# Optimization experiments

Measured on AMD Instinct MI355X. Metric: run time of the kernel, lower is better.

## Reference

```python
import jax, jax.numpy as jnp
import numpy as np

N_POINTS = 32
N_HEADS = 4
EMBED = 256
TAU = 2.0


def _grid_sample_bilinear(val, gx, gy):
    # val: [N, C, H, W]; gx, gy: [N, Q, P] normalized coords in [-1, 1]
    # bilinear, padding_mode='zeros', align_corners=False
    N, C, H, W = val.shape
    ix = (gx + 1.0) * (W * 0.5) - 0.5
    iy = (gy + 1.0) * (H * 0.5) - 0.5
    x0 = jnp.floor(ix)
    y0 = jnp.floor(iy)
    x1 = x0 + 1.0
    y1 = y0 + 1.0
    wx1 = ix - x0
    wx0 = 1.0 - wx1
    wy1 = iy - y0
    wy0 = 1.0 - wy1
    gather = jax.vmap(lambda v, yy, xx: v[:, yy, xx])  # per-image advanced-index gather
    out = jnp.zeros((N, C) + gx.shape[1:], dtype=val.dtype)
    for xs, ys, wx, wy in ((x0, y0, wx0, wy0), (x1, y0, wx1, wy0),
                           (x0, y1, wx0, wy1), (x1, y1, wx1, wy1)):
        m = ((xs >= 0) & (xs < W) & (ys >= 0) & (ys < H)).astype(val.dtype) * wx * wy
        xi = jnp.clip(xs, 0, W - 1).astype(jnp.int32)
        yi = jnp.clip(ys, 0, H - 1).astype(jnp.int32)
        out = out + gather(val, yi, xi) * m[:, None]
    return out  # [N, C, Q, P]


def setup_inputs() -> dict:
    key = jax.random.key(0)
    ks = jax.random.split(key, 18)
    B, L = 2, 1000
    lvl_hw = [(256, 256), (128, 128), (64, 64), (32, 32)]
    inp = {}
    for i, (h, w) in enumerate(lvl_hw):
        inp[f'value{i}'] = jax.random.normal(ks[i], (B, EMBED, h, w), jnp.float32)
    inp['query_content'] = jax.random.normal(ks[4], (B, L, EMBED), jnp.float32)
    img = 1024.0
    xy = jax.random.uniform(ks[5], (B, L, 2), minval=0.0, maxval=img)
    z = jax.random.uniform(ks[6], (B, L, 1), minval=4.0, maxval=6.5)
    r = jax.random.uniform(ks[7], (B, L, 1), minval=-0.8, maxval=0.8)
    th = jax.random.uniform(ks[8], (B, L, 1), minval=-np.pi, maxval=np.pi)
    inp['query_xyzrt'] = jnp.concatenate([xy, z, r, th], axis=-1).astype(jnp.float32)
    inp['strides'] = jnp.array([4, 8, 16, 32], jnp.int32)
    s = 0.02
    inp['W_off'] = jax.random.normal(ks[9], (EMBED, N_HEADS * N_POINTS * 3)) * s
    inp['b_off'] = jax.random.normal(ks[10], (N_HEADS * N_POINTS * 3,)) * 0.2
    inp['W_ca1'] = jax.random.normal(ks[11], (EMBED, EMBED // 4)) * s
    inp['W_ca2'] = jax.random.normal(ks[12], (EMBED // 4, EMBED)) * s
    inp['W_sa1'] = jax.random.normal(ks[13], (EMBED, EMBED // 4)) * s
    inp['W_sa2'] = jax.random.normal(ks[14], (EMBED // 4, N_HEADS * N_POINTS)) * s
    inp['W_out'] = jax.random.normal(ks[15], (EMBED * N_POINTS, EMBED)) * s
    inp['b_out'] = jnp.zeros((EMBED,), jnp.float32)
    return inp


def reference(value0, value1, value2, value3, query_content, query_xyzrt, strides,
              W_off, b_off, W_ca1, W_ca2, W_sa1, W_sa2, W_out, b_out):
    values = [value0, value1, value2, value3]
    B, L, _ = query_content.shape
    P = N_HEADS * N_POINTS
    G = N_HEADS
    ch = EMBED // G

    # ---- make_sample_points ----
    offset = (query_content @ W_off + b_off).reshape(B, L, P, 3)
    roi_cc = query_xyzrt[..., :2]                      # [B,L,2]
    scale = 2.0 ** query_xyzrt[..., 2:3]
    ratio = 2.0 ** jnp.concatenate([query_xyzrt[..., 3:4] * -0.5,
                                    query_xyzrt[..., 3:4] * 0.5], axis=-1)
    roi_wh = scale * ratio                             # [B,L,2]
    theta = query_xyzrt[..., 4]
    c, s = jnp.cos(theta), jnp.sin(theta)
    R = jnp.stack([jnp.stack([c, -s], -1), jnp.stack([s, c], -1)], -2)  # [B,L,2,2]
    off_xy = offset[..., :2] * roi_wh[:, :, None, :]
    rot_xy = jnp.einsum('blpj,blij->blpi', off_xy, R)  # offset @ R^T
    sample_xy = roi_cc[:, :, None, :] + rot_xy         # [B,L,P,2] absolute coords
    sample_z = query_xyzrt[..., 2][:, :, None] + offset[..., 2]  # [B,L,P]

    # ---- level weights: sigmoid(-(z - log2(stride))^2 / tau) ----
    grid = jnp.log2(strides.astype(sample_z.dtype))    # [n_levels]
    lvl_w = jax.nn.sigmoid(-((sample_z[..., None] - grid) ** 2) / TAU)  # [B,L,P,n_lvl]

    # ---- multi-level rotated deformable sampling ----
    sampling_value = jnp.zeros((B, L, G, N_POINTS, ch), query_content.dtype)
    for lvl, v in enumerate(values):
        H, W = v.shape[2], v.shape[3]
        stride_f = strides[lvl].astype(sample_xy.dtype)
        mapping = jnp.stack([W * stride_f, H * stride_f])  # (x_extent, y_extent)
        norm_xy = sample_xy / mapping * 2.0 - 1.0          # [B,L,P,2] in [-1,1]
        # split points into head groups: [B,L,G,pts,2] -> [B*G, L, pts, 2]
        g_xy = norm_xy.reshape(B, L, G, N_POINTS, 2).transpose(0, 2, 1, 3, 4).reshape(B * G, L, N_POINTS, 2)
        v_g = v.reshape(B * G, ch, H, W)
        out = _grid_sample_bilinear(v_g, g_xy[..., 0], g_xy[..., 1])  # [B*G, ch, L, pts]
        w = lvl_w[..., lvl].reshape(B, L, G, N_POINTS).transpose(0, 2, 1, 3).reshape(B * G, 1, L, N_POINTS)
        out = out * w
        sampling_value = sampling_value + out.reshape(B, G, ch, L, N_POINTS).transpose(0, 3, 1, 4, 2)

    # ---- channel / spatial attention gates ----
    ca = jax.nn.sigmoid(jax.nn.relu(query_content @ W_ca1) @ W_ca2)
    ca = ca.reshape(B, L, G, 1, ch)
    sa = jax.nn.sigmoid(jax.nn.relu(query_content @ W_sa1) @ W_sa2)
    sa = sa.reshape(B, L, G, N_POINTS, 1)
    out = sampling_value * ca * sa
    out = out.reshape(B, L, G * N_POINTS * ch) @ W_out + b_out
    return out + query_content
```

## Files before the change

### kernel.cpp

```cpp
#include <hip/hip_runtime.h>

#define NQ    2000
#define KDIM  8192
#define EMB   256
#define MPAD  2048
#define SPLITK 8

typedef __attribute__((ext_vector_type(8))) short bf16x8;
typedef __attribute__((ext_vector_type(4))) float f32x4;

__device__ __forceinline__ float sigf(float x) { return 1.0f / (1.0f + __expf(-x)); }

__device__ __forceinline__ unsigned short f2bf(float x) {
    union { float f; unsigned int u; } v; v.f = x;
    unsigned int r = v.u + 0x7fffu + ((v.u >> 16) & 1u);
    return (unsigned short)(r >> 16);
}
__device__ __forceinline__ float bf2f(unsigned short h) {
    union { unsigned int u; float f; } v; v.u = ((unsigned int)h) << 16; return v.f;
}

__global__ __launch_bounds__(256) void trans_kernel(
    const float* __restrict__ v0, const float* __restrict__ v1,
    const float* __restrict__ v2, const float* __restrict__ v3,
    unsigned short* __restrict__ vt0, unsigned short* __restrict__ vt1,
    unsigned short* __restrict__ vt2, unsigned short* __restrict__ vt3,
    const float* __restrict__ Wout, unsigned short* __restrict__ Wtb,
    const float* __restrict__ Woff, const float* __restrict__ Wca1,
    const float* __restrict__ Wsa1,
    unsigned short* __restrict__ WH, unsigned short* __restrict__ WL,
    const float* __restrict__ qc,
    unsigned short* __restrict__ qcH, unsigned short* __restrict__ qcL)
{
    __shared__ float tile[64][33];
    int bid = blockIdx.x;
    const int t = threadIdx.x;

    if (bid < 21760) {
        const float* v; unsigned short* vt; int H;
        if (bid < 16384)      { v = v0; vt = vt0; H = 256; }
        else if (bid < 20480) { bid -= 16384; v = v1; vt = vt1; H = 128; }
        else if (bid < 21504) { bid -= 20480; v = v2; vt = vt2; H = 64; }
        else                  { bid -= 21504; v = v3; vt = vt3; H = 32; }
        const int y  = bid % H;            bid /= H;
        const int xt = bid % (H >> 5);     bid /= (H >> 5);
        const int ct = bid & 3;
        const int b  = bid >> 2;
        const float* src = v + ((size_t)(b * 256 + ct * 64) * H + y) * H + xt * 32;
        const int xi = t & 31;
        #pragma unroll
        for (int i = 0; i < 8; i++) {
            const int c = (t >> 5) + i * 8;
            tile[c][xi] = src[(size_t)c * H * H + xi];
        }
        __syncthreads();
        unsigned short* dst = vt + (((size_t)(b * H + y) * H + xt * 32) * 256) + ct * 64;
        const int ci = (t & 31) * 2;
        #pragma unroll
        for (int i = 0; i < 4; i++) {
            const int x2 = (t >> 5) + i * 8;
            ushort2 pk;
            pk.x = f2bf(tile[ci][x2]);
            pk.y = f2bf(tile[ci + 1][x2]);
            *(ushort2*)(dst + (size_t)x2 * 256 + ci) = pk;
        }
    } else if (bid < 23808) {
        const int local = bid - 21760;
        const int k0 = (local & 255) * 32, n0 = (local >> 8) * 32;
        float (*tl)[33] = tile;
        #pragma unroll
        for (int i = 0; i < 4; i++) {
            const int ki = (t >> 5) + i * 8;
            tl[ki][t & 31] = Wout[(size_t)(k0 + ki) * 256 + n0 + (t & 31)];
        }
        __syncthreads();
        #pragma unroll
        for (int i = 0; i < 4; i++) {
            const int ni = (t >> 5) + i * 8;
            const int ki = t & 31;
            Wtb[(size_t)(n0 + ni) * KDIM + k0 + ki] = f2bf(tl[ki][ni]);
        }
    } else if (bid < 24320) {
        const int n = bid - 23808;
        float val;
        if (n < 384)      val = Woff[(size_t)t * 384 + n];
        else if (n < 448) val = Wca1[(size_t)t * 64 + (n - 384)];
        else              val = Wsa1[(size_t)t * 64 + (n - 448)];
        const unsigned short hh = f2bf(val);
        WH[(size_t)n * 256 + t] = hh;
        WL[(size_t)n * 256 + t] = f2bf(val - bf2f(hh));
    } else {
        const int q = bid - 24320;
        const float val = (q < NQ) ? qc[(size_t)q * 256 + t] : 0.f;
        const unsigned short hh = f2bf(val);
        qcH[(size_t)q * 256 + t] = hh;
        qcL[(size_t)q * 256 + t] = f2bf(val - bf2f(hh));
    }
}

__global__ __launch_bounds__(256) void gemmA_kernel(
    const unsigned short* __restrict__ qcH, const unsigned short* __restrict__ qcL,
    const unsigned short* __restrict__ WH,  const unsigned short* __restrict__ WL,
    float* __restrict__ Hout)
{
    const int m0 = blockIdx.x * 64;
    const int n0 = blockIdx.y * 64;
    const int t  = threadIdx.x;
    const int w    = t >> 6;
    const int lane = t & 63;
    const int mw = (w & 1) * 32;
    const int nw = (w >> 1) * 32;
    const int quad = lane >> 4;
    const int l16  = lane & 15;

    f32x4 acc[2][2] = {};
    #pragma unroll
    for (int pass = 0; pass < 3; pass++) {
        const unsigned short* Ap = (pass == 2) ? qcL : qcH;
        const unsigned short* Bp = (pass == 1) ? WL : WH;
        const unsigned short* ar0 = Ap + (size_t)(m0 + mw + l16) * 256 + quad * 8;
        const unsigned short* ar1 = ar0 + 16 * 256;
        const unsigned short* br0 = Bp + (size_t)(n0 + nw + l16) * 256 + quad * 8;
        const unsigned short* br1 = br0 + 16 * 256;
        #pragma unroll
        for (int k = 0; k < 256; k += 32) {
            const bf16x8 a0 = *(const bf16x8*)(ar0 + k);
            const bf16x8 a1 = *(const bf16x8*)(ar1 + k);
            const bf16x8 b0 = *(const bf16x8*)(br0 + k);
            const bf16x8 b1 = *(const bf16x8*)(br1 + k);
            acc[0][0] = __builtin_amdgcn_mfma_f32_16x16x32_bf16(a0, b0, acc[0][0], 0, 0, 0);
            acc[0][1] = __builtin_amdgcn_mfma_f32_16x16x32_bf16(a0, b1, acc[0][1], 0, 0, 0);
            acc[1][0] = __builtin_amdgcn_mfma_f32_16x16x32_bf16(a1, b0, acc[1][0], 0, 0, 0);
            acc[1][1] = __builtin_amdgcn_mfma_f32_16x16x32_bf16(a1, b1, acc[1][1], 0, 0, 0);
        }
    }
    #pragma unroll
    for (int i = 0; i < 2; i++)
        #pragma unroll
        for (int j = 0; j < 2; j++) {
            const int n = n0 + nw + 16 * j + l16;
            #pragma unroll
            for (int r = 0; r < 4; r++) {
                const int m = m0 + mw + 16 * i + quad * 4 + r;
                Hout[(size_t)m * 512 + n] = acc[i][j][r];
            }
        }
}

__global__ __launch_bounds__(256) void finish_kernel(
    const float* __restrict__ Hbuf, const float* __restrict__ xyzrt,
    const float* __restrict__ boff,
    const float* __restrict__ Wca2, const float* __restrict__ Wsa2,
    float* __restrict__ qdata)
{
    const int q0 = blockIdx.x * 8;
    const int t  = threadIdx.x;
    __shared__ float hca[8][64];
    __shared__ float hsa[8][64];
    __shared__ float sas[8][128];

    for (int i = t; i < 1024; i += 256) {
        const int q = i >> 7, j = i & 127;
        const float v = fmaxf(Hbuf[(size_t)(q0 + q) * 512 + 384 + j], 0.f);
        if (j < 64) hca[q][j] = v; else hsa[q][j - 64] = v;
    }
    __syncthreads();

    {
        float acc[8] = {};
        for (int j = 0; j < 64; j++) {
            const float wv = Wca2[(size_t)j * 256 + t];
            #pragma unroll
            for (int q = 0; q < 8; q++) acc[q] = fmaf(hca[q][j], wv, acc[q]);
        }
        #pragma unroll
        for (int q = 0; q < 8; q++)
            qdata[(size_t)(q0 + q) * 1024 + 768 + t] = sigf(acc[q]);
    }
    {
        const int c  = t & 127;
        const int qb = (t >> 7) * 4;
        float acc[4] = {};
        for (int j = 0; j < 64; j++) {
            const float wv = Wsa2[(size_t)j * 128 + c];
            #pragma unroll
            for (int qq = 0; qq < 4; qq++) acc[qq] = fmaf(hsa[qb + qq][j], wv, acc[qq]);
        }
        #pragma unroll
        for (int qq = 0; qq < 4; qq++) sas[qb + qq][c] = sigf(acc[qq]);
    }
    __syncthreads();

    {
        const int p  = t & 127;
        const int qb = (t >> 7) * 4;
        #pragma unroll
        for (int qq = 0; qq < 4; qq++) {
            const int q = qb + qq;
            const float* hrow = Hbuf + (size_t)(q0 + q) * 512 + p * 3;
            const float o0 = hrow[0] + boff[p * 3 + 0];
            const float o1 = hrow[1] + boff[p * 3 + 1];
            const float o2 = hrow[2] + boff[p * 3 + 2];
            const float* xr = xyzrt + (size_t)(q0 + q) * 5;
            const float x = xr[0], y = xr[1], z = xr[2], r = xr[3], th = xr[4];
            const float sc  = exp2f(z);
            const float rw  = sc * exp2f(-0.5f * r);
            const float rh  = sc * exp2f( 0.5f * r);
            const float cth = __cosf(th), sth = __sinf(th);
            const float ox = o0 * rw;
            const float oy = o1 * rh;
            float* qd = qdata + (size_t)(q0 + q) * 1024;
            qd[p]       = x + cth * ox - sth * oy;
            qd[128 + p] = y + sth * ox + cth * oy;
            const float sz = z + o2;
            const float sa = sas[q][p];
            #pragma unroll
            for (int l = 0; l < 4; l++) {
                const float d = sz - (float)(2 + l);
                qd[256 + p * 4 + l] = sigf(-0.5f * d * d) * sa;
            }
        }
    }
}

__global__ __launch_bounds__(256) void sample_kernel(
    const unsigned short* __restrict__ v0, const unsigned short* __restrict__ v1,
    const unsigned short* __restrict__ v2, const unsigned short* __restrict__ v3,
    const float* __restrict__ qdata,
    unsigned short* __restrict__ X)
{
    const int wid  = blockIdx.x * 4 + (threadIdx.x >> 6);
    const int lane = threadIdx.x & 63;
    const int q  = wid >> 4;
    const int pb = (wid & 15) * 8;
    const int pt = lane >> 3;
    const int gp = pb + pt;
    const int g  = gp >> 5;
    const int c8 = (lane & 7) * 8;
    const int b  = (q >= 1000) ? 1 : 0;

    const float* qd = qdata + (size_t)q * 1024;
    const float px = qd[gp];
    const float py = qd[128 + gp];
    float wlv[4];
    #pragma unroll
    for (int l = 0; l < 4; l++) wlv[l] = qd[256 + gp * 4 + l];

    const unsigned short* vals[4] = { v0, v1, v2, v3 };
    const int cbase = g * 64 + c8;

    float acc[8] = {};
    #pragma unroll
    for (int l = 0; l < 4; l++) {
        const int   H   = 256 >> l;
        const float inv = 1.0f / (float)(4 << l);
        const float wl  = wlv[l];
        const float ix = px * inv - 0.5f;
        const float iy = py * inv - 0.5f;
        const float x0f = floorf(ix), y0f = floorf(iy);
        const int   x0 = (int)x0f,    y0 = (int)y0f;
        const float fx1 = ix - x0f, fx0 = 1.f - fx1;
        const float fy1 = iy - y0f, fy0 = 1.f - fy1;
        const bool xi0 = (x0 >= 0) & (x0 < H);
        const bool xi1 = (x0 + 1 >= 0) & (x0 + 1 < H);
        const bool yi0 = (y0 >= 0) & (y0 < H);
        const bool yi1 = (y0 + 1 >= 0) & (y0 + 1 < H);
        const int xc0 = min(max(x0, 0), H - 1);
        const int xc1 = min(max(x0 + 1, 0), H - 1);
        const int yc0 = min(max(y0, 0), H - 1);
        const int yc1 = min(max(y0 + 1, 0), H - 1);
        const float m00 = (xi0 & yi0) ? wl * fx0 * fy0 : 0.f;
        const float m10 = (xi1 & yi0) ? wl * fx1 * fy0 : 0.f;
        const float m01 = (xi0 & yi1) ? wl * fx0 * fy1 : 0.f;
        const float m11 = (xi1 & yi1) ? wl * fx1 * fy1 : 0.f;

        const unsigned short* base = vals[l] + (size_t)b * H * H * 256 + cbase;
        const int ry0 = yc0 * H, ry1 = yc1 * H;
        const uint4 d00 = *(const uint4*)(base + (size_t)(ry0 + xc0) * 256);
        const uint4 d10 = *(const uint4*)(base + (size_t)(ry0 + xc1) * 256);
        const uint4 d01 = *(const uint4*)(base + (size_t)(ry1 + xc0) * 256);
        const uint4 d11 = *(const uint4*)(base + (size_t)(ry1 + xc1) * 256);

        const uint4 dv[4] = { d00, d10, d01, d11 };
        const float mv[4] = { m00, m10, m01, m11 };
        #pragma unroll
        for (int tap = 0; tap < 4; tap++) {
            const unsigned int du[4] = { dv[tap].x, dv[tap].y, dv[tap].z, dv[tap].w };
            const float m = mv[tap];
            #pragma unroll
            for (int i = 0; i < 4; i++) {
                union { unsigned int u; float f; } lo, hi;
                lo.u = du[i] << 16;
                hi.u = du[i] & 0xffff0000u;
                acc[2 * i]     = fmaf(m, lo.f, acc[2 * i]);
                acc[2 * i + 1] = fmaf(m, hi.f, acc[2 * i + 1]);
            }
        }
    }

    const float* caf = qd + 768 + cbase;
    const float4 ca0 = *(const float4*)caf;
    const float4 ca1 = *(const float4*)(caf + 4);
    const float cav[8] = { ca0.x, ca0.y, ca0.z, ca0.w, ca1.x, ca1.y, ca1.z, ca1.w };
    uint4 o;
    unsigned int* op = (unsigned int*)&o;
    #pragma unroll
    for (int i = 0; i < 4; i++) {
        const unsigned int lo = f2bf(acc[2 * i] * cav[2 * i]);
        const unsigned int hi = f2bf(acc[2 * i + 1] * cav[2 * i + 1]);
        op[i] = lo | (hi << 16);
    }
    *(uint4*)(X + (size_t)q * KDIM + pb * 64 + lane * 8) = o;
}

__global__ __launch_bounds__(256) void gemm_kernel(
    const unsigned short* __restrict__ X,
    const unsigned short* __restrict__ Wt,
    float* __restrict__ part)
{
    const int m0 = blockIdx.x * 64;
    const int n0 = blockIdx.y * 64;
    const int z  = blockIdx.z;
    const int t  = threadIdx.x;
    const int w    = t >> 6;
    const int lane = t & 63;
    const int mw = (w & 1) * 32;
    const int nw = (w >> 1) * 32;
    const int quad = lane >> 4;
    const int l16  = lane & 15;

    const unsigned short* ar0 = X  + (size_t)(m0 + mw + l16) * KDIM + quad * 8;
    const unsigned short* ar1 = ar0 + (size_t)16 * KDIM;
    const unsigned short* br0 = Wt + (size_t)(n0 + nw + l16) * KDIM + quad * 8;
    const unsigned short* br1 = br0 + (size_t)16 * KDIM;

    f32x4 acc[2][2] = {};
    const int kbase = z * (KDIM / SPLITK);
    #pragma unroll 4
    for (int k = kbase; k < kbase + KDIM / SPLITK; k += 32) {
        const bf16x8 a0 = *(const bf16x8*)(ar0 + k);
        const bf16x8 a1 = *(const bf16x8*)(ar1 + k);
        const bf16x8 b0 = *(const bf16x8*)(br0 + k);
        const bf16x8 b1 = *(const bf16x8*)(br1 + k);
        acc[0][0] = __builtin_amdgcn_mfma_f32_16x16x32_bf16(a0, b0, acc[0][0], 0, 0, 0);
        acc[0][1] = __builtin_amdgcn_mfma_f32_16x16x32_bf16(a0, b1, acc[0][1], 0, 0, 0);
        acc[1][0] = __builtin_amdgcn_mfma_f32_16x16x32_bf16(a1, b0, acc[1][0], 0, 0, 0);
        acc[1][1] = __builtin_amdgcn_mfma_f32_16x16x32_bf16(a1, b1, acc[1][1], 0, 0, 0);
    }

    float* pz = part + (size_t)z * MPAD * EMB;
    #pragma unroll
    for (int i = 0; i < 2; i++)
        #pragma unroll
        for (int j = 0; j < 2; j++) {
            const int n = n0 + nw + 16 * j + l16;
            #pragma unroll
            for (int r = 0; r < 4; r++) {
                const int m = m0 + mw + 16 * i + quad * 4 + r;
                pz[(size_t)m * EMB + n] = acc[i][j][r];
            }
        }
}

__global__ __launch_bounds__(256) void reduce_kernel(
    const float* __restrict__ part, const float* __restrict__ qc,
    const float* __restrict__ bias, float* __restrict__ out)
{
    const int idx = blockIdx.x * 256 + threadIdx.x;
    if (idx >= NQ * 64) return;
    const int m  = idx >> 6;
    const int c4 = idx & 63;
    float4 a = ((const float4*)bias)[c4];
    const float4 qv = ((const float4*)qc)[(size_t)m * 64 + c4];
    a.x += qv.x; a.y += qv.y; a.z += qv.z; a.w += qv.w;
    #pragma unroll
    for (int z = 0; z < SPLITK; z++) {
        const float4 p = ((const float4*)part)[((size_t)z * MPAD + m) * 64 + c4];
        a.x += p.x; a.y += p.y; a.z += p.z; a.w += p.w;
    }
    ((float4*)out)[(size_t)m * 64 + c4] = a;
}

extern "C" void kernel_launch(void* const* d_in, const int* in_sizes, int n_in,
                              void* d_out, int out_size, void* d_ws, size_t ws_size,
                              hipStream_t stream) {
    (void)in_sizes; (void)n_in; (void)out_size; (void)ws_size;
    const float* v0    = (const float*)d_in[0];
    const float* v1    = (const float*)d_in[1];
    const float* v2    = (const float*)d_in[2];
    const float* v3    = (const float*)d_in[3];
    const float* qc    = (const float*)d_in[4];
    const float* xyzrt = (const float*)d_in[5];
    const float* Woff  = (const float*)d_in[7];
    const float* boff  = (const float*)d_in[8];
    const float* Wca1  = (const float*)d_in[9];
    const float* Wca2  = (const float*)d_in[10];
    const float* Wsa1  = (const float*)d_in[11];
    const float* Wsa2  = (const float*)d_in[12];
    const float* Wout  = (const float*)d_in[13];
    const float* bout  = (const float*)d_in[14];
    float* out = (float*)d_out;

    char* p = (char*)d_ws;
    float* qdata = (float*)p;                 p += (size_t)NQ * 1024 * 4;
    unsigned short* Xb = (unsigned short*)p;  p += (size_t)MPAD * KDIM * 2;
    unsigned short* vt0 = (unsigned short*)p; p += (size_t)2 * 256 * 256 * 256 * 2;
    unsigned short* vt1 = (unsigned short*)p; p += (size_t)2 * 128 * 128 * 256 * 2;
    unsigned short* vt2 = (unsigned short*)p; p += (size_t)2 * 64 * 64 * 256 * 2;
    unsigned short* vt3 = (unsigned short*)p; p += (size_t)2 * 32 * 32 * 256 * 2;
    unsigned short* Wtb = (unsigned short*)p; p += (size_t)EMB * KDIM * 2;
    float* partb = (float*)p;                 p += (size_t)SPLITK * MPAD * EMB * 4;
    float* Hbuf = (float*)p;                  p += (size_t)MPAD * 512 * 4;
    unsigned short* qcH = (unsigned short*)p; p += (size_t)MPAD * 256 * 2;
    unsigned short* qcL = (unsigned short*)p; p += (size_t)MPAD * 256 * 2;
    unsigned short* WHb = (unsigned short*)p; p += (size_t)512 * 256 * 2;
    unsigned short* WLb = (unsigned short*)p;

    trans_kernel<<<26368, 256, 0, stream>>>(v0, v1, v2, v3, vt0, vt1, vt2, vt3,
                                            Wout, Wtb, Woff, Wca1, Wsa1,
                                            WHb, WLb, qc, qcH, qcL);
    gemmA_kernel<<<dim3(MPAD / 64, 8), 256, 0, stream>>>(qcH, qcL, WHb, WLb, Hbuf);
    finish_kernel<<<NQ / 8, 256, 0, stream>>>(Hbuf, xyzrt, boff, Wca2, Wsa2, qdata);
    sample_kernel<<<(NQ * 128) / (4 * 8), 256, 0, stream>>>(vt0, vt1, vt2, vt3, qdata, Xb);
    gemm_kernel<<<dim3(MPAD / 64, EMB / 64, SPLITK), 256, 0, stream>>>(Xb, Wtb, partb);
    reduce_kernel<<<(NQ * 64 + 255) / 256, 256, 0, stream>>>(partb, qc, bout, out);
}
```

Measured before the change: 388.8 us.

## Widen value transpose tiles, vectorize bf16 packing, batch sampling loads per level pair

The value transpose for levels 0-2 now uses 64x64 tiles with float4 global loads and 16-byte bf16 stores, halving the block count. Level 3 keeps its own 32-wide path. Packing uses the hardware bf16x2 conversion intrinsic. The sampling kernel issues the eight gathers of two levels before the FMAs, to get more loads in flight, and accumulates in float2 vectors to encourage packed FMA. The cost is more register pressure and a larger LDS tile.

```diff
diff --git a/kernel.cpp b/kernel.cpp
--- a/kernel.cpp
+++ b/kernel.cpp
@@ -1,4 +1,5 @@
 #include <hip/hip_runtime.h>
+#include <hip/hip_bf16.h>
 
 #define NQ    2000
 #define KDIM  8192
@@ -8,6 +9,7 @@
 
 typedef __attribute__((ext_vector_type(8))) short bf16x8;
 typedef __attribute__((ext_vector_type(4))) float f32x4;
+typedef __attribute__((ext_vector_type(2))) float f32x2;
 
 __device__ __forceinline__ float sigf(float x) { return 1.0f / (1.0f + __expf(-x)); }
 
@@ -18,6 +20,11 @@
 }
 __device__ __forceinline__ float bf2f(unsigned short h) {
     union { unsigned int u; float f; } v; v.u = ((unsigned int)h) << 16; return v.f;
+}
+__device__ __forceinline__ unsigned int pkbf(float lo, float hi) {
+    __hip_bfloat162 b = __float22bfloat162_rn(make_float2(lo, hi));
+    union { __hip_bfloat162 b2; unsigned int u; } c; c.b2 = b;
+    return c.u;
 }
 
 __global__ __launch_bounds__(256) void trans_kernel(
@@ -32,56 +39,82 @@
     const float* __restrict__ qc,
     unsigned short* __restrict__ qcH, unsigned short* __restrict__ qcL)
 {
-    __shared__ float tile[64][33];
+    __shared__ float tile[64][68];
     int bid = blockIdx.x;
     const int t = threadIdx.x;
 
-    if (bid < 21760) {
-        const float* v; unsigned short* vt; int H;
-        if (bid < 16384)      { v = v0; vt = vt0; H = 256; }
-        else if (bid < 20480) { bid -= 16384; v = v1; vt = vt1; H = 128; }
-        else if (bid < 21504) { bid -= 20480; v = v2; vt = vt2; H = 64; }
-        else                  { bid -= 21504; v = v3; vt = vt3; H = 32; }
-        const int y  = bid % H;            bid /= H;
-        const int xt = bid % (H >> 5);     bid /= (H >> 5);
-        const int ct = bid & 3;
-        const int b  = bid >> 2;
-        const float* src = v + ((size_t)(b * 256 + ct * 64) * H + y) * H + xt * 32;
+    if (bid < 10752) {
+        const float* v; unsigned short* vt; int H; int local;
+        if (bid < 8192)       { v = v0; vt = vt0; H = 256; local = bid; }
+        else if (bid < 10240) { v = v1; vt = vt1; H = 128; local = bid - 8192; }
+        else                  { v = v2; vt = vt2; H = 64;  local = bid - 10240; }
+        const int y  = local % H;          local /= H;
+        const int xt = local % (H >> 6);   local /= (H >> 6);
+        const int ct = local & 3;
+        const int b  = local >> 2;
+
+        const int c  = t >> 2;
+        const int xq = (t & 3) * 16;
+        const float* src = v + ((size_t)(b * 256 + ct * 64 + c) * H + y) * H + xt * 64 + xq;
+        #pragma unroll
+        for (int i = 0; i < 4; i++) {
+            const float4 f = ((const float4*)src)[i];
+            *(float4*)&tile[c][xq + 4 * i] = f;
+        }
+        __syncthreads();
+
+        const int x  = t >> 2;
+        const int cq = (t & 3) * 16;
+        unsigned short* dst = vt + (((size_t)(b * H + y) * H + xt * 64 + x) * 256) + ct * 64 + cq;
+        #pragma unroll
+        for (int half = 0; half < 2; half++) {
+            uint4 o;
+            unsigned int* op = (unsigned int*)&o;
+            #pragma unroll
+            for (int j = 0; j < 4; j++) {
+                const int cc = cq + half * 8 + 2 * j;
+                op[j] = pkbf(tile[cc][x], tile[cc + 1][x]);
+            }
+            *(uint4*)(dst + half * 8) = o;
+        }
+    } else if (bid < 11008) {
+        int local = bid - 10752;
+        const int y  = local & 31;  local >>= 5;
+        const int ct = local & 3;
+        const int b  = local >> 2;
+        const float* src = v3 + ((size_t)(b * 256 + ct * 64) * 32 + y) * 32;
         const int xi = t & 31;
         #pragma unroll
         for (int i = 0; i < 8; i++) {
             const int c = (t >> 5) + i * 8;
-            tile[c][xi] = src[(size_t)c * H * H + xi];
+            tile[c][xi] = src[(size_t)c * 32 * 32 + xi];
         }
         __syncthreads();
-        unsigned short* dst = vt + (((size_t)(b * H + y) * H + xt * 32) * 256) + ct * 64;
+        unsigned short* dst = vt3 + (((size_t)(b * 32 + y) * 32) * 256) + ct * 64;
         const int ci = (t & 31) * 2;
         #pragma unroll
         for (int i = 0; i < 4; i++) {
             const int x2 = (t >> 5) + i * 8;
-            ushort2 pk;
-            pk.x = f2bf(tile[ci][x2]);
-            pk.y = f2bf(tile[ci + 1][x2]);
-            *(ushort2*)(dst + (size_t)x2 * 256 + ci) = pk;
-        }
-    } else if (bid < 23808) {
-        const int local = bid - 21760;
+            *(unsigned int*)(dst + (size_t)x2 * 256 + ci) = pkbf(tile[ci][x2], tile[ci + 1][x2]);
+        }
+    } else if (bid < 13056) {
+        const int local = bid - 11008;
         const int k0 = (local & 255) * 32, n0 = (local >> 8) * 32;
-        float (*tl)[33] = tile;
+        float* tl = &tile[0][0];
         #pragma unroll
         for (int i = 0; i < 4; i++) {
             const int ki = (t >> 5) + i * 8;
-            tl[ki][t & 31] = Wout[(size_t)(k0 + ki) * 256 + n0 + (t & 31)];
+            tl[ki * 33 + (t & 31)] = Wout[(size_t)(k0 + ki) * 256 + n0 + (t & 31)];
         }
         __syncthreads();
         #pragma unroll
         for (int i = 0; i < 4; i++) {
             const int ni = (t >> 5) + i * 8;
             const int ki = t & 31;
-            Wtb[(size_t)(n0 + ni) * KDIM + k0 + ki] = f2bf(tl[ki][ni]);
-        }
-    } else if (bid < 24320) {
-        const int n = bid - 23808;
+            Wtb[(size_t)(n0 + ni) * KDIM + k0 + ki] = f2bf(tl[ki * 33 + ni]);
+        }
+    } else if (bid < 13568) {
+        const int n = bid - 13056;
         float val;
         if (n < 384)      val = Woff[(size_t)t * 384 + n];
         else if (n < 448) val = Wca1[(size_t)t * 64 + (n - 384)];
@@ -90,7 +123,7 @@
         WH[(size_t)n * 256 + t] = hh;
         WL[(size_t)n * 256 + t] = f2bf(val - bf2f(hh));
     } else {
-        const int q = bid - 24320;
+        const int q = bid - 13568;
         const float val = (q < NQ) ? qc[(size_t)q * 256 + t] : 0.f;
         const unsigned short hh = f2bf(val);
         qcH[(size_t)q * 256 + t] = hh;
@@ -242,58 +275,60 @@
     const float* qd = qdata + (size_t)q * 1024;
     const float px = qd[gp];
     const float py = qd[128 + gp];
-    float wlv[4];
-    #pragma unroll
-    for (int l = 0; l < 4; l++) wlv[l] = qd[256 + gp * 4 + l];
+    const float4 wl4 = *(const float4*)(qd + 256 + gp * 4);
+    const float wlv[4] = { wl4.x, wl4.y, wl4.z, wl4.w };
 
     const unsigned short* vals[4] = { v0, v1, v2, v3 };
     const int cbase = g * 64 + c8;
 
-    float acc[8] = {};
-    #pragma unroll
-    for (int l = 0; l < 4; l++) {
-        const int   H   = 256 >> l;
-        const float inv = 1.0f / (float)(4 << l);
-        const float wl  = wlv[l];
-        const float ix = px * inv - 0.5f;
-        const float iy = py * inv - 0.5f;
-        const float x0f = floorf(ix), y0f = floorf(iy);
-        const int   x0 = (int)x0f,    y0 = (int)y0f;
-        const float fx1 = ix - x0f, fx0 = 1.f - fx1;
-        const float fy1 = iy - y0f, fy0 = 1.f - fy1;
-        const bool xi0 = (x0 >= 0) & (x0 < H);
-        const bool xi1 = (x0 + 1 >= 0) & (x0 + 1 < H);
-        const bool yi0 = (y0 >= 0) & (y0 < H);
-        const bool yi1 = (y0 + 1 >= 0) & (y0 + 1 < H);
-        const int xc0 = min(max(x0, 0), H - 1);
-        const int xc1 = min(max(x0 + 1, 0), H - 1);
-        const int yc0 = min(max(y0, 0), H - 1);
-        const int yc1 = min(max(y0 + 1, 0), H - 1);
-        const float m00 = (xi0 & yi0) ? wl * fx0 * fy0 : 0.f;
-        const float m10 = (xi1 & yi0) ? wl * fx1 * fy0 : 0.f;
-        const float m01 = (xi0 & yi1) ? wl * fx0 * fy1 : 0.f;
-        const float m11 = (xi1 & yi1) ? wl * fx1 * fy1 : 0.f;
-
-        const unsigned short* base = vals[l] + (size_t)b * H * H * 256 + cbase;
-        const int ry0 = yc0 * H, ry1 = yc1 * H;
-        const uint4 d00 = *(const uint4*)(base + (size_t)(ry0 + xc0) * 256);
-        const uint4 d10 = *(const uint4*)(base + (size_t)(ry0 + xc1) * 256);
-        const uint4 d01 = *(const uint4*)(base + (size_t)(ry1 + xc0) * 256);
-        const uint4 d11 = *(const uint4*)(base + (size_t)(ry1 + xc1) * 256);
-
-        const uint4 dv[4] = { d00, d10, d01, d11 };
-        const float mv[4] = { m00, m10, m01, m11 };
-        #pragma unroll
-        for (int tap = 0; tap < 4; tap++) {
-            const unsigned int du[4] = { dv[tap].x, dv[tap].y, dv[tap].z, dv[tap].w };
-            const float m = mv[tap];
-            #pragma unroll
-            for (int i = 0; i < 4; i++) {
+    f32x2 acc2[4] = {};
+    #pragma unroll
+    for (int h = 0; h < 2; h++) {
+        uint4 d[8];
+        float m[8];
+        #pragma unroll
+        for (int li = 0; li < 2; li++) {
+            const int l = h * 2 + li;
+            const int   H   = 256 >> l;
+            const float inv = 1.0f / (float)(4 << l);
+            const float wl  = wlv[l];
+            const float ix = px * inv - 0.5f;
+            const float iy = py * inv - 0.5f;
+            const float x0f = floorf(ix), y0f = floorf(iy);
+            const int   x0 = (int)x0f,    y0 = (int)y0f;
+            const float fx1 = ix - x0f, fx0 = 1.f - fx1;
+            const float fy1 = iy - y0f, fy0 = 1.f - fy1;
+            const bool xi0 = (x0 >= 0) & (x0 < H);
+            const bool xi1 = (x0 + 1 >= 0) & (x0 + 1 < H);
+            const bool yi0 = (y0 >= 0) & (y0 < H);
+            const bool yi1 = (y0 + 1 >= 0) & (y0 + 1 < H);
+            const int xc0 = min(max(x0, 0), H - 1);
+            const int xc1 = min(max(x0 + 1, 0), H - 1);
+            const int yc0 = min(max(y0, 0), H - 1);
+            const int yc1 = min(max(y0 + 1, 0), H - 1);
+            m[li * 4 + 0] = (xi0 & yi0) ? wl * fx0 * fy0 : 0.f;
+            m[li * 4 + 1] = (xi1 & yi0) ? wl * fx1 * fy0 : 0.f;
+            m[li * 4 + 2] = (xi0 & yi1) ? wl * fx0 * fy1 : 0.f;
+            m[li * 4 + 3] = (xi1 & yi1) ? wl * fx1 * fy1 : 0.f;
+
+            const unsigned short* base = vals[l] + (size_t)b * H * H * 256 + cbase;
+            const int ry0 = yc0 * H, ry1 = yc1 * H;
+            d[li * 4 + 0] = *(const uint4*)(base + (size_t)(ry0 + xc0) * 256);
+            d[li * 4 + 1] = *(const uint4*)(base + (size_t)(ry0 + xc1) * 256);
+            d[li * 4 + 2] = *(const uint4*)(base + (size_t)(ry1 + xc0) * 256);
+            d[li * 4 + 3] = *(const uint4*)(base + (size_t)(ry1 + xc1) * 256);
+        }
+        #pragma unroll
+        for (int i = 0; i < 8; i++) {
+            const unsigned int du[4] = { d[i].x, d[i].y, d[i].z, d[i].w };
+            const f32x2 mv = { m[i], m[i] };
+            #pragma unroll
+            for (int j = 0; j < 4; j++) {
                 union { unsigned int u; float f; } lo, hi;
-                lo.u = du[i] << 16;
-                hi.u = du[i] & 0xffff0000u;
-                acc[2 * i]     = fmaf(m, lo.f, acc[2 * i]);
-                acc[2 * i + 1] = fmaf(m, hi.f, acc[2 * i + 1]);
+                lo.u = du[j] << 16;
+                hi.u = du[j] & 0xffff0000u;
+                f32x2 t2 = { lo.f, hi.f };
+                acc2[j] = acc2[j] + mv * t2;
             }
         }
     }
@@ -301,14 +336,14 @@
     const float* caf = qd + 768 + cbase;
     const float4 ca0 = *(const float4*)caf;
     const float4 ca1 = *(const float4*)(caf + 4);
-    const float cav[8] = { ca0.x, ca0.y, ca0.z, ca0.w, ca1.x, ca1.y, ca1.z, ca1.w };
+    const f32x2 cav[4] = { { ca0.x, ca0.y }, { ca0.z, ca0.w },
+                           { ca1.x, ca1.y }, { ca1.z, ca1.w } };
     uint4 o;
     unsigned int* op = (unsigned int*)&o;
     #pragma unroll
-    for (int i = 0; i < 4; i++) {
-        const unsigned int lo = f2bf(acc[2 * i] * cav[2 * i]);
-        const unsigned int hi = f2bf(acc[2 * i + 1] * cav[2 * i + 1]);
-        op[i] = lo | (hi << 16);
+    for (int j = 0; j < 4; j++) {
+        const f32x2 r = acc2[j] * cav[j];
+        op[j] = pkbf(r.x, r.y);
     }
     *(uint4*)(X + (size_t)q * KDIM + pb * 64 + lane * 8) = o;
 }
@@ -416,7 +451,7 @@
     unsigned short* WHb = (unsigned short*)p; p += (size_t)512 * 256 * 2;
     unsigned short* WLb = (unsigned short*)p;
 
-    trans_kernel<<<26368, 256, 0, stream>>>(v0, v1, v2, v3, vt0, vt1, vt2, vt3,
+    trans_kernel<<<15616, 256, 0, stream>>>(v0, v1, v2, v3, vt0, vt1, vt2, vt3,
                                             Wout, Wtb, Woff, Wca1, Wsa1,
                                             WHb, WLb, qc, qcH, qcL);
     gemmA_kernel<<<dim3(MPAD / 64, 8), 256, 0, stream>>>(qcH, qcL, WHb, WLb, Hbuf);
```

After: 389.9 us. About the same (+0.3%).
